# Performance work log

Measured on AMD Instinct MI355X. Metric: run time of the kernel, lower is better.

The kernel has to match this reference:

```python
import jax, jax.numpy as jnp
import numpy as np

N = 4096      # nodes
F = 32        # num_features (GATConv in = out per head)
H = 2         # heads
NHID = 64     # per-branch mlp output
C = 10        # num_classes
J = 3         # wavelet filters
E = 65536     # edges (avg degree 16)
G = 13        # num_gat = (3**3 - 1) // 2
NEG_SLOPE = 0.2


def setup_inputs() -> dict:
    key = jax.random.key(0)
    ks = jax.random.split(key, 12)
    sc = np.float32(1.0 / np.sqrt(N))
    g = np.float32(0.1)
    x = jax.random.normal(ks[0], (N, F), jnp.float32)
    edge_index = jax.random.randint(ks[1], (2, E), 0, N)
    U = jax.random.normal(ks[2], (N, N), jnp.float32) * sc
    psi = jax.random.normal(ks[3], (J, N, N), jnp.float32) * sc
    # 13 GATConv(F, F, heads=H) parameter stacks
    gat_W = jax.random.normal(ks[4], (G, F, H * F), jnp.float32) * g
    att_src = jax.random.normal(ks[5], (G, H, F), jnp.float32) * g
    att_dst = jax.random.normal(ks[6], (G, H, F), jnp.float32) * g
    gat_b = jnp.zeros((G, H * F), jnp.float32)
    # 13 branch MLPs: Linear(H*F -> NHID)
    mlp_W = jax.random.normal(ks[7], (G, H * F, NHID), jnp.float32) * g
    mlp_b = jnp.zeros((G, NHID), jnp.float32)
    # final head: Linear(13*NHID -> C)
    out_W = jax.random.normal(ks[8], (G * NHID, C), jnp.float32) * g
    out_b = jnp.zeros((C,), jnp.float32)
    return {"x": x, "edge_index": edge_index, "U": U, "psi": psi,
            "gat_W": gat_W, "att_src": att_src, "att_dst": att_dst,
            "gat_b": gat_b, "mlp_W": mlp_W, "mlp_b": mlp_b,
            "out_W": out_W, "out_b": out_b}


def _gat_branch(coef, W, a_s, a_d, bg, mw, mb, src, dst):
    # GATConv(F, F, heads=H, concat=True) in eval mode, then ELU + Linear.
    h = (coef @ W).reshape(N, H, F)                       # [N,H,F]
    es = jnp.einsum('nhf,hf->nh', h, a_s)                 # src attention logits
    ed = jnp.einsum('nhf,hf->nh', h, a_d)                 # dst attention logits
    e = jax.nn.leaky_relu(es[src] + ed[dst], NEG_SLOPE)   # [E+N,H]
    m = jax.ops.segment_max(e, dst, num_segments=N)       # stable softmax per dst
    w = jnp.exp(e - m[dst])
    z = jax.ops.segment_sum(w, dst, num_segments=N)
    alpha = w / (z[dst] + 1e-16)
    out = jax.ops.segment_sum(alpha[:, :, None] * h[src], dst, num_segments=N)
    out = out.reshape(N, H * F) + bg
    return jax.nn.elu(out) @ mw + mb                      # branch MLP -> [N,NHID]


def reference(x, edge_index, U, psi, gat_W, att_src, att_dst, gat_b,
              mlp_W, mlp_b, out_W, out_b):
    loops = jnp.arange(N)
    src = jnp.concatenate([edge_index[0], loops])         # add_self_loops
    dst = jnp.concatenate([edge_index[1], loops])
    # Scattering tree (layer=3, J=3): 1 + 3 + 9 = 13 coefficient maps.
    af = jnp.abs(x)
    coef0 = U @ af                                        # [N,F]
    y1 = jnp.einsum('jnm,mf->jnf', psi, af)               # level-1 wavelets [J,N,F]
    a1 = jnp.abs(y1)
    coef1 = jnp.einsum('nm,jmf->jnf', U, a1)              # [J,N,F]
    y2 = jnp.einsum('knm,jmf->jknf', psi, a1)             # level-2: psi_k @ |y1_j|
    coef2 = jnp.einsum('nm,jkmf->jknf', U, jnp.abs(y2)).reshape(J * J, N, F)
    coefs = jnp.concatenate([coef0[None], coef1, coef2], axis=0)  # [13,N,F]
    branch = jax.vmap(lambda c, W, a_s, a_d, bg, mw, mb:
                      _gat_branch(c, W, a_s, a_d, bg, mw, mb, src, dst))
    yb = branch(coefs, gat_W, att_src, att_dst, gat_b, mlp_W, mlp_b)  # [13,N,NHID]
    feat = jnp.moveaxis(yb, 0, 1).reshape(N, G * NHID)    # concat branches per node
    logits = jax.nn.elu(feat) @ out_W + out_b             # [N,C]
    return jax.nn.log_softmax(logits, axis=1)
```

## Files before the change

kernel.cpp:

```cpp
#include <hip/hip_runtime.h>
#include <hip/hip_bf16.h>

#define NN 4096
#define FF 32
#define EE 65536
#define GG 13

typedef float floatx4 __attribute__((ext_vector_type(4)));
typedef __bf16 bf16x8 __attribute__((ext_vector_type(8)));
typedef short short8 __attribute__((ext_vector_type(8)));

__device__ inline unsigned short f2bf(float f) {
    unsigned u = __float_as_uint(f);
    u += 0x7FFFu + ((u >> 16) & 1u);
    return (unsigned short)(u >> 16);
}


__global__ void k_prep1(const float* __restrict__ x, unsigned short* __restrict__ B) {
    int tid = blockIdx.x * 256 + threadIdx.x;
    int k = tid >> 5, col = tid & 31;
    float v = fabsf(x[tid]);
    B[(((k >> 5) * 2 + (col >> 4)) << 9) + ((col & 15) << 5) + (k & 31)] = f2bf(v);
}

__global__ void k_prep2(const float* __restrict__ P1, unsigned short* __restrict__ B) {
    int tid = blockIdx.x * 256 + threadIdx.x;
    int k = tid / 96, jf = tid % 96;
    int j = jf >> 5, f = jf & 31;
    float v = fabsf(P1[((1 + j) * NN + k) * FF + f]);
    B[(((k >> 5) * 6 + (jf >> 4)) << 9) + ((jf & 15) << 5) + (k & 31)] = f2bf(v);
}

__global__ void k_prep3(const float* __restrict__ P2, unsigned short* __restrict__ B) {
    int tid = blockIdx.x * 256 + threadIdx.x;
    int k = tid / 288, cc = tid % 288;
    int k3 = cc / 96, jf = cc % 96;
    float v = fabsf(P2[((1 + k3) * NN + k) * 96 + jf]);
    B[(((k >> 5) * 18 + (cc >> 4)) << 9) + ((cc & 15) << 5) + (k & 31)] = f2bf(v);
}

template <int NT>
__global__ __launch_bounds__(512) void k_pass(const float* __restrict__ Umat,
                                              const float* __restrict__ Psi,
                                              const unsigned short* __restrict__ Bfrag,
                                              float* __restrict__ Pout) {
    constexpr int NC = NT * 16;
    int tile = blockIdx.x;
    int mat = blockIdx.y;
    const float* A = (mat == 0) ? Umat : (Psi + (size_t)(mat - 1) * NN * NN);
    int tid = threadIdx.x;
    int wave = tid >> 6, lane = tid & 63;
    int c15 = lane & 15, q = lane >> 4;
    int row = tile * 16 + c15;
    const float* arow = A + (size_t)row * NN + wave * 512 + q * 8;
    const unsigned short* bbase = Bfrag + (size_t)(wave * 16) * NT * 512 + (c15 << 5) + (q << 3);

    floatx4 acc[NT];
#pragma unroll
    for (int t = 0; t < NT; t++) acc[t] = (floatx4){0.f, 0.f, 0.f, 0.f};

    for (int s = 0; s < 16; s++) {
        const float* ap = arow + s * 32;
        floatx4 a0 = *(const floatx4*)ap;
        floatx4 a1 = *(const floatx4*)(ap + 4);
        short8 av;
        av[0] = f2bf(a0[0]); av[1] = f2bf(a0[1]); av[2] = f2bf(a0[2]); av[3] = f2bf(a0[3]);
        av[4] = f2bf(a1[0]); av[5] = f2bf(a1[1]); av[6] = f2bf(a1[2]); av[7] = f2bf(a1[3]);
        bf16x8 ab = __builtin_bit_cast(bf16x8, av);
        const unsigned short* bp = bbase + (size_t)s * NT * 512;
#pragma unroll
        for (int t = 0; t < NT; t++) {
            short8 bv = *(const short8*)(bp + t * 512);
            acc[t] = __builtin_amdgcn_mfma_f32_16x16x32_bf16(
                ab, __builtin_bit_cast(bf16x8, bv), acc[t], 0, 0, 0);
        }
    }

    __shared__ float cs[16 * NC];
    for (int w = 0; w < 8; w++) {
        if (wave == w) {
#pragma unroll
            for (int t = 0; t < NT; t++)
#pragma unroll
                for (int r = 0; r < 4; r++) {
                    int idx = (q * 4 + r) * NC + t * 16 + c15;
                    if (w == 0) cs[idx] = acc[t][r]; else cs[idx] += acc[t][r];
                }
        }
        __syncthreads();
    }
    float* orow = Pout + ((size_t)mat * NN + (size_t)tile * 16) * NC;
    for (int i = tid; i < 16 * NC; i += 512) orow[i] = cs[i];
}

__global__ void k_h(const float* __restrict__ P1, const float* __restrict__ P2,
                    const float* __restrict__ P3, const float* __restrict__ gatW,
                    float* __restrict__ h) {
    int tid = blockIdx.x * 256 + threadIdx.x;
    int g = tid >> 18;
    int n = (tid & ((1 << 18) - 1)) >> 6;
    int hc = tid & 63;
    const float* crow;
    if (g == 0) crow = P1 + (size_t)n * FF;
    else if (g <= 3) crow = P2 + (size_t)n * 96 + (g - 1) * 32;
    else {
        int j = (g - 4) / 3, k3 = (g - 4) % 3;
        crow = P3 + (size_t)n * 288 + k3 * 96 + j * 32;
    }
    const float* wcol = gatW + g * (32 * 64) + hc;
    float a = 0.f;
#pragma unroll
    for (int f = 0; f < 32; f++) a += crow[f] * wcol[f * 64];
    h[tid] = a;
}

__global__ void k_esed(const float* __restrict__ h, const float* __restrict__ attS,
                       const float* __restrict__ attD, float* __restrict__ es,
                       float* __restrict__ ed) {
    int tid = blockIdx.x * 256 + threadIdx.x;
    int g = tid >> 12;
    const float* hrow = h + (size_t)tid * 64;
    const float* as = attS + g * 64;
    const float* ad = attD + g * 64;
    float e0 = 0, e1 = 0, d0 = 0, d1 = 0;
#pragma unroll
    for (int i = 0; i < 32; i++) {
        float v0 = hrow[i], v1 = hrow[32 + i];
        e0 += v0 * as[i];      e1 += v1 * as[32 + i];
        d0 += v0 * ad[i];      d1 += v1 * ad[32 + i];
    }
    es[tid * 2] = e0; es[tid * 2 + 1] = e1;
    ed[tid * 2] = d0; ed[tid * 2 + 1] = d1;
}

__global__ void k_hist(const int* __restrict__ ei, int* __restrict__ cnt) {
    int e = blockIdx.x * 256 + threadIdx.x;
    int d = (e < EE) ? ei[EE + e] : (e - EE);
    atomicAdd(&cnt[d], 1);
}

__global__ void k_scan(const int* __restrict__ cnt, int* __restrict__ offs,
                       int* __restrict__ cursor) {
    int lane = threadIdx.x;
    int base = lane * 64;
    int s = 0;
    for (int i = 0; i < 64; i++) s += cnt[base + i];
    int x = s;
    for (int d = 1; d < 64; d <<= 1) {
        int y = __shfl_up(x, d);
        if (lane >= d) x += y;
    }
    int run = x - s;
    for (int i = 0; i < 64; i++) {
        offs[base + i] = run;
        cursor[base + i] = run;
        run += cnt[base + i];
    }
}

__global__ void k_scatter(const int* __restrict__ ei, int* __restrict__ cursor,
                          int* __restrict__ csr) {
    int e = blockIdx.x * 256 + threadIdx.x;
    int s, d;
    if (e < EE) { s = ei[e]; d = ei[EE + e]; } else { s = d = e - EE; }
    int pos = atomicAdd(&cursor[d], 1);
    csr[pos] = s;
}

__global__ void k_gat(const float* __restrict__ h, const float* __restrict__ es,
                      const float* __restrict__ ed, const int* __restrict__ offs,
                      const int* __restrict__ cnt, const int* __restrict__ csr,
                      const float* __restrict__ gatb, float* __restrict__ gact) {
    int w = (blockIdx.x * 256 + threadIdx.x) >> 6;
    int lane = threadIdx.x & 63, hh = lane >> 5;
    int g = w >> 12, n = w & 4095;
    float myed = ed[w * 2 + hh];
    int start = offs[n], deg = cnt[n];
    const float* hg = h + (size_t)g * NN * 64;
    const float* esg = es + (size_t)g * NN * 2;
    float m = -INFINITY, z = 0.f, acc = 0.f;
    for (int i = 0; i < deg; i++) {
        int s = csr[start + i];
        float lg = esg[s * 2 + hh] + myed;
        lg = (lg > 0.f) ? lg : 0.2f * lg;
        float nm = fmaxf(m, lg);
        float sc = __expf(m - nm);
        float we = __expf(lg - nm);
        z = z * sc + we;
        acc = acc * sc + we * hg[(size_t)s * 64 + lane];
        m = nm;
    }
    float o = acc / (z + 1e-16f) + gatb[g * 64 + lane];
    o = (o > 0.f) ? o : (__expf(o) - 1.f);
    gact[(size_t)w * 64 + lane] = o;
}

__global__ void k_mlp(const float* __restrict__ gact, const float* __restrict__ mlpW,
                      const float* __restrict__ mlpb, float* __restrict__ feat) {
    int tid = blockIdx.x * 256 + threadIdx.x;
    int g = tid >> 18;
    int n = (tid & ((1 << 18) - 1)) >> 6;
    int k = tid & 63;
    const float* grow = gact + ((size_t)g * NN + n) * 64;
    const float* wc = mlpW + (size_t)g * 64 * 64 + k;
    float a = mlpb[g * 64 + k];
#pragma unroll 8
    for (int i = 0; i < 64; i++) a += grow[i] * wc[i * 64];
    a = (a > 0.f) ? a : (__expf(a) - 1.f);
    feat[(size_t)n * 832 + g * 64 + k] = a;
}

__global__ void k_final(const float* __restrict__ feat, const float* __restrict__ oW,
                        const float* __restrict__ ob, float* __restrict__ out) {
    int w = (blockIdx.x * 256 + threadIdx.x) >> 6;
    int lane = threadIdx.x & 63;
    float a[10];
#pragma unroll
    for (int c = 0; c < 10; c++) a[c] = 0.f;
    const float* frow = feat + (size_t)w * 832;
#pragma unroll
    for (int i = 0; i < 13; i++) {
        float v = frow[i * 64 + lane];
        const float* wp = oW + (i * 64 + lane) * 10;
#pragma unroll
        for (int c = 0; c < 10; c++) a[c] += v * wp[c];
    }
#pragma unroll
    for (int off = 32; off >= 1; off >>= 1)
#pragma unroll
        for (int c = 0; c < 10; c++) a[c] += __shfl_down(a[c], off);
    if (lane == 0) {
        float m = -INFINITY;
#pragma unroll
        for (int c = 0; c < 10; c++) { a[c] += ob[c]; m = fmaxf(m, a[c]); }
        float s = 0.f;
#pragma unroll
        for (int c = 0; c < 10; c++) s += __expf(a[c] - m);
        float lse = m + __logf(s);
#pragma unroll
        for (int c = 0; c < 10; c++) out[w * 10 + c] = a[c] - lse;
    }
}

extern "C" void kernel_launch(void* const* d_in, const int* in_sizes, int n_in,
                              void* d_out, int out_size, void* d_ws, size_t ws_size,
                              hipStream_t stream) {
    const float* x    = (const float*)d_in[0];
    const int*   ei   = (const int*)d_in[1];
    const float* U    = (const float*)d_in[2];
    const float* psi  = (const float*)d_in[3];
    const float* gatW = (const float*)d_in[4];
    const float* attS = (const float*)d_in[5];
    const float* attD = (const float*)d_in[6];
    const float* gatb = (const float*)d_in[7];
    const float* mlpW = (const float*)d_in[8];
    const float* mlpb = (const float*)d_in[9];
    const float* oW   = (const float*)d_in[10];
    const float* ob   = (const float*)d_in[11];
    float* out = (float*)d_out;

    char* ws = (char*)d_ws;
    size_t off = 0;
    auto alloc = [&](size_t bytes) { char* p = ws + off; off += (bytes + 255) & ~(size_t)255; return p; };
    unsigned short* bf1 = (unsigned short*)alloc((size_t)NN * 32 * 2);
    float* P1           = (float*)alloc((size_t)4 * NN * 32 * 4);
    unsigned short* bf2 = (unsigned short*)alloc((size_t)NN * 96 * 2);
    float* P2           = (float*)alloc((size_t)4 * NN * 96 * 4);
    unsigned short* bf3 = (unsigned short*)alloc((size_t)NN * 288 * 2);
    float* P3           = (float*)alloc((size_t)NN * 288 * 4);
    float* h            = (float*)alloc((size_t)GG * NN * 64 * 4);
    float* es           = (float*)alloc((size_t)GG * NN * 2 * 4);
    float* ed           = (float*)alloc((size_t)GG * NN * 2 * 4);
    int* cnt            = (int*)alloc((size_t)NN * 4);
    int* offs           = (int*)alloc((size_t)NN * 4);
    int* cursor         = (int*)alloc((size_t)NN * 4);
    int* csr            = (int*)alloc((size_t)(EE + NN) * 4);
    float* gact         = (float*)alloc((size_t)GG * NN * 64 * 4);
    float* feat         = (float*)alloc((size_t)NN * 832 * 4);
    (void)ws_size; (void)in_sizes; (void)n_in; (void)out_size;

    hipMemsetAsync(cnt, 0, NN * 4, stream);
    k_hist<<<(EE + NN) / 256, 256, 0, stream>>>(ei, cnt);
    k_scan<<<1, 64, 0, stream>>>(cnt, offs, cursor);
    k_scatter<<<(EE + NN) / 256, 256, 0, stream>>>(ei, cursor, csr);

    k_prep1<<<(NN * 32) / 256, 256, 0, stream>>>(x, bf1);
    k_pass<2><<<dim3(NN / 16, 4), 512, 0, stream>>>(U, psi, bf1, P1);
    k_prep2<<<(NN * 96) / 256, 256, 0, stream>>>(P1, bf2);
    k_pass<6><<<dim3(NN / 16, 4), 512, 0, stream>>>(U, psi, bf2, P2);
    k_prep3<<<(NN * 288) / 256, 256, 0, stream>>>(P2, bf3);
    k_pass<18><<<dim3(NN / 16, 1), 512, 0, stream>>>(U, psi, bf3, P3);

    k_h<<<(GG * NN * 64) / 256, 256, 0, stream>>>(P1, P2, P3, gatW, h);
    k_esed<<<(GG * NN) / 256, 256, 0, stream>>>(h, attS, attD, es, ed);
    k_gat<<<(GG * NN * 64) / 256, 256, 0, stream>>>(h, es, ed, offs, cnt, csr, gatb, gact);
    k_mlp<<<(GG * NN * 64) / 256, 256, 0, stream>>>(gact, mlpW, mlpb, feat);
    k_final<<<(NN * 64) / 256, 256, 0, stream>>>(feat, oW, ob, out);
}
```

Baseline: 721.7 us.

## Prefetch A/B and edge loads, fuse h with attention logits, halve reduction syncs

The dense pass kernel now software-pipelines the next A row chunk and batches the B fragment loads before the MFMA chain. Its cross-wave reduction uses two shared buffers, cutting the serialized sync rounds from eight to four. The separate h and es/ed kernels are fused, with the attention dot products done by warp shuffles. The GAT edge loop prefetches neighbor indices and features two steps ahead to hide gather latency. This costs more registers and LDS per block, and the k_gat prefetch reads csr[start] even when the degree is zero, though self-loops make that safe.

Measured after the change: 670.2 us. -7.1%, faster.

```diff
diff --git a/kernel.cpp b/kernel.cpp
--- a/kernel.cpp
+++ b/kernel.cpp
@@ -60,47 +60,57 @@
 #pragma unroll
     for (int t = 0; t < NT; t++) acc[t] = (floatx4){0.f, 0.f, 0.f, 0.f};
 
+    floatx4 a0 = *(const floatx4*)arow;
+    floatx4 a1 = *(const floatx4*)(arow + 4);
+
     for (int s = 0; s < 16; s++) {
-        const float* ap = arow + s * 32;
-        floatx4 a0 = *(const floatx4*)ap;
-        floatx4 a1 = *(const floatx4*)(ap + 4);
+        const unsigned short* bp = bbase + (size_t)s * NT * 512;
+        short8 bv[NT];
+#pragma unroll
+        for (int t = 0; t < NT; t++) bv[t] = *(const short8*)(bp + t * 512);
+        floatx4 n0 = {}, n1 = {};
+        if (s < 15) {
+            n0 = *(const floatx4*)(arow + (s + 1) * 32);
+            n1 = *(const floatx4*)(arow + (s + 1) * 32 + 4);
+        }
         short8 av;
         av[0] = f2bf(a0[0]); av[1] = f2bf(a0[1]); av[2] = f2bf(a0[2]); av[3] = f2bf(a0[3]);
         av[4] = f2bf(a1[0]); av[5] = f2bf(a1[1]); av[6] = f2bf(a1[2]); av[7] = f2bf(a1[3]);
         bf16x8 ab = __builtin_bit_cast(bf16x8, av);
-        const unsigned short* bp = bbase + (size_t)s * NT * 512;
-#pragma unroll
-        for (int t = 0; t < NT; t++) {
-            short8 bv = *(const short8*)(bp + t * 512);
+#pragma unroll
+        for (int t = 0; t < NT; t++)
             acc[t] = __builtin_amdgcn_mfma_f32_16x16x32_bf16(
-                ab, __builtin_bit_cast(bf16x8, bv), acc[t], 0, 0, 0);
-        }
-    }
-
-    __shared__ float cs[16 * NC];
-    for (int w = 0; w < 8; w++) {
-        if (wave == w) {
+                ab, __builtin_bit_cast(bf16x8, bv[t]), acc[t], 0, 0, 0);
+        a0 = n0; a1 = n1;
+    }
+
+    __shared__ float cs[2][16 * NC];
+    int half = wave & 1;
+    for (int w2 = 0; w2 < 4; w2++) {
+        if ((wave >> 1) == w2) {
 #pragma unroll
             for (int t = 0; t < NT; t++)
 #pragma unroll
                 for (int r = 0; r < 4; r++) {
                     int idx = (q * 4 + r) * NC + t * 16 + c15;
-                    if (w == 0) cs[idx] = acc[t][r]; else cs[idx] += acc[t][r];
+                    if (w2 == 0) cs[half][idx] = acc[t][r];
+                    else cs[half][idx] += acc[t][r];
                 }
         }
         __syncthreads();
     }
     float* orow = Pout + ((size_t)mat * NN + (size_t)tile * 16) * NC;
-    for (int i = tid; i < 16 * NC; i += 512) orow[i] = cs[i];
-}
-
-__global__ void k_h(const float* __restrict__ P1, const float* __restrict__ P2,
-                    const float* __restrict__ P3, const float* __restrict__ gatW,
-                    float* __restrict__ h) {
-    int tid = blockIdx.x * 256 + threadIdx.x;
-    int g = tid >> 18;
-    int n = (tid & ((1 << 18) - 1)) >> 6;
-    int hc = tid & 63;
+    for (int i = tid; i < 16 * NC; i += 512) orow[i] = cs[0][i] + cs[1][i];
+}
+
+__global__ void k_hes(const float* __restrict__ P1, const float* __restrict__ P2,
+                      const float* __restrict__ P3, const float* __restrict__ gatW,
+                      const float* __restrict__ attS, const float* __restrict__ attD,
+                      float* __restrict__ h, float* __restrict__ es,
+                      float* __restrict__ ed) {
+    int w = (blockIdx.x * 256 + threadIdx.x) >> 6;
+    int lane = threadIdx.x & 63;
+    int g = w >> 12, n = w & 4095;
     const float* crow;
     if (g == 0) crow = P1 + (size_t)n * FF;
     else if (g <= 3) crow = P2 + (size_t)n * 96 + (g - 1) * 32;
@@ -108,30 +118,22 @@
         int j = (g - 4) / 3, k3 = (g - 4) % 3;
         crow = P3 + (size_t)n * 288 + k3 * 96 + j * 32;
     }
-    const float* wcol = gatW + g * (32 * 64) + hc;
+    const float* wcol = gatW + g * (32 * 64) + lane;
     float a = 0.f;
 #pragma unroll
     for (int f = 0; f < 32; f++) a += crow[f] * wcol[f * 64];
-    h[tid] = a;
-}
-
-__global__ void k_esed(const float* __restrict__ h, const float* __restrict__ attS,
-                       const float* __restrict__ attD, float* __restrict__ es,
-                       float* __restrict__ ed) {
-    int tid = blockIdx.x * 256 + threadIdx.x;
-    int g = tid >> 12;
-    const float* hrow = h + (size_t)tid * 64;
-    const float* as = attS + g * 64;
-    const float* ad = attD + g * 64;
-    float e0 = 0, e1 = 0, d0 = 0, d1 = 0;
-#pragma unroll
-    for (int i = 0; i < 32; i++) {
-        float v0 = hrow[i], v1 = hrow[32 + i];
-        e0 += v0 * as[i];      e1 += v1 * as[32 + i];
-        d0 += v0 * ad[i];      d1 += v1 * ad[32 + i];
-    }
-    es[tid * 2] = e0; es[tid * 2 + 1] = e1;
-    ed[tid * 2] = d0; ed[tid * 2 + 1] = d1;
+    h[(size_t)w * 64 + lane] = a;
+    float vs = a * attS[g * 64 + lane];
+    float vd = a * attD[g * 64 + lane];
+#pragma unroll
+    for (int off = 16; off >= 1; off >>= 1) {
+        vs += __shfl_down(vs, off, 32);
+        vd += __shfl_down(vd, off, 32);
+    }
+    if ((lane & 31) == 0) {
+        es[w * 2 + (lane >> 5)] = vs;
+        ed[w * 2 + (lane >> 5)] = vd;
+    }
 }
 
 __global__ void k_hist(const int* __restrict__ ei, int* __restrict__ cnt) {
@@ -176,22 +178,30 @@
     int lane = threadIdx.x & 63, hh = lane >> 5;
     int g = w >> 12, n = w & 4095;
     float myed = ed[w * 2 + hh];
+    float bias = gatb[g * 64 + lane];
     int start = offs[n], deg = cnt[n];
     const float* hg = h + (size_t)g * NN * 64;
     const float* esg = es + (size_t)g * NN * 2;
+    int sA = csr[start];
+    int sB = (deg > 1) ? csr[start + 1] : 0;
+    float hvA = hg[(size_t)sA * 64 + lane];
+    float lgA = esg[sA * 2 + hh];
     float m = -INFINITY, z = 0.f, acc = 0.f;
     for (int i = 0; i < deg; i++) {
-        int s = csr[start + i];
-        float lg = esg[s * 2 + hh] + myed;
+        int sC = (i + 2 < deg) ? csr[start + i + 2] : 0;
+        float hvB = hg[(size_t)sB * 64 + lane];
+        float lgB = esg[sB * 2 + hh];
+        float lg = lgA + myed;
         lg = (lg > 0.f) ? lg : 0.2f * lg;
         float nm = fmaxf(m, lg);
         float sc = __expf(m - nm);
         float we = __expf(lg - nm);
         z = z * sc + we;
-        acc = acc * sc + we * hg[(size_t)s * 64 + lane];
+        acc = acc * sc + we * hvA;
         m = nm;
-    }
-    float o = acc / (z + 1e-16f) + gatb[g * 64 + lane];
+        sA = sB; sB = sC; hvA = hvB; lgA = lgB;
+    }
+    float o = acc / (z + 1e-16f) + bias;
     o = (o > 0.f) ? o : (__expf(o) - 1.f);
     gact[(size_t)w * 64 + lane] = o;
 }
@@ -292,8 +302,7 @@
     k_prep3<<<(NN * 288) / 256, 256, 0, stream>>>(P2, bf3);
     k_pass<18><<<dim3(NN / 16, 1), 512, 0, stream>>>(U, psi, bf3, P3);
 
-    k_h<<<(GG * NN * 64) / 256, 256, 0, stream>>>(P1, P2, P3, gatW, h);
-    k_esed<<<(GG * NN) / 256, 256, 0, stream>>>(h, attS, attD, es, ed);
+    k_hes<<<(GG * NN * 64) / 256, 256, 0, stream>>>(P1, P2, P3, gatW, attS, attD, h, es, ed);
     k_gat<<<(GG * NN * 64) / 256, 256, 0, stream>>>(h, es, ed, offs, cnt, csr, gatb, gact);
     k_mlp<<<(GG * NN * 64) / 256, 256, 0, stream>>>(gact, mlpW, mlpb, feat);
     k_final<<<(NN * 64) / 256, 256, 0, stream>>>(feat, oW, ob, out);
```
